# Optimization experiments

Hardware: AMD Instinct MI355X
Metric: run time of the kernel (lower is better)

The kernel has to match this reference:

```python
import jax, jax.numpy as jnp
import numpy as np

# Render constants matching GaussianRenderer(__init__): image size and top-K blend depth.
H, W, K = 128, 128, 10
N_G = 2048  # number of gaussians


def setup_inputs() -> dict:
    key = jax.random.key(0)
    k1, k2, k3, k4 = jax.random.split(key, 4)
    # Means in pixel coordinates so gaussians cover the image.
    gaussian_means = jax.random.uniform(k1, (N_G, 2), dtype=jnp.float32) * jnp.array([W, H], jnp.float32)
    # Rotation angle per gaussian in [0, 2pi).
    gaussian_rotations = jax.random.uniform(k2, (N_G,), dtype=jnp.float32) * (2.0 * np.pi)
    # log std-devs centered at log(3) => ~3px footprint.
    gaussian_log_scales = jax.random.normal(k3, (N_G, 2), dtype=jnp.float32) * 0.3 + np.log(3.0)
    gaussian_colors = jax.random.uniform(k4, (N_G, 3), dtype=jnp.float32)
    return {
        "gaussian_means": gaussian_means,
        "gaussian_rotations": gaussian_rotations,
        "gaussian_log_scales": gaussian_log_scales,
        "gaussian_colors": gaussian_colors,
    }


def reference(gaussian_means, gaussian_rotations, gaussian_log_scales, gaussian_colors):
    """2D Gaussian splatting: per-pixel top-K gaussians by opacity, alpha-composited.

    Covariance per gaussian: Sigma = R(theta) diag(exp(2*log_scales)) R(theta)^T.
    alpha_i(p) = exp(-0.5 * d^T Sigma^{-1} d), d = p - mean_i.
    Per pixel, the K gaussians with largest alpha are blended front-to-back:
        out = sum_i color_i * alpha_i * prod_{j<i} (1 - alpha_j).
    (The torch module's tile binning + max_G_per_tile is a GPU performance
    optimization; the dense evaluation here computes the same per-pixel math.)
    """
    cos_t = jnp.cos(gaussian_rotations)  # [N]
    sin_t = jnp.sin(gaussian_rotations)
    inv_var = jnp.exp(-2.0 * gaussian_log_scales)  # [N,2] = 1/sigma^2 per axis
    ivx, ivy = inv_var[:, 0], inv_var[:, 1]
    # Sigma^{-1} = R diag(1/sx^2, 1/sy^2) R^T  (symmetric 2x2: [[a, b], [b, c]])
    a = cos_t * cos_t * ivx + sin_t * sin_t * ivy  # [N]
    c = sin_t * sin_t * ivx + cos_t * cos_t * ivy
    b = cos_t * sin_t * (ivx - ivy)

    xs = jnp.arange(W, dtype=jnp.float32) + 0.5
    ys = jnp.arange(H, dtype=jnp.float32) + 0.5
    px, py = jnp.meshgrid(xs, ys)  # [H,W] each
    dx = px.reshape(-1, 1) - gaussian_means[:, 0]  # [P, N], P = H*W
    dy = py.reshape(-1, 1) - gaussian_means[:, 1]
    q = a * dx * dx + 2.0 * b * dx * dy + c * dy * dy  # Mahalanobis distance^2 [P,N]
    alpha = jnp.exp(-0.5 * q)  # [P,N] in (0,1]

    top_alpha, top_idx = jax.lax.top_k(alpha, K)  # [P,K], descending alpha
    # Front-to-back transmittance: T_0 = 1, T_i = prod_{j<i} (1 - alpha_j)
    trans = jnp.cumprod(1.0 - top_alpha, axis=1)
    trans = jnp.concatenate([jnp.ones_like(trans[:, :1]), trans[:, :-1]], axis=1)
    weight = top_alpha * trans  # [P,K]
    top_colors = gaussian_colors[top_idx]  # [P,K,3]
    image = jnp.einsum("pk,pkc->pc", weight, top_colors).reshape(H, W, 3)
    return image
```

## Files before the change

### kernel.cpp

```cpp
#include <hip/hip_runtime.h>

#define HH 128
#define WW 128
#define NPX (HH * WW)
#define KK 10
#define PXB 16
#define LCAP 352
#define JMAX 22
#define KEYC 6
#define SCAP (16 * KEYC)
#define SPAD (SCAP + 1)
#define ALPHA_MIN 5e-4f
#define RADIUS_K 3.8990f

typedef unsigned long long u64;
typedef unsigned int u32;

__global__ __launch_bounds__(256) void precompute_kernel(
    const float* __restrict__ means, const float* __restrict__ rots,
    const float* __restrict__ lscales, int nG,
    float4* __restrict__ bbox4, float4* __restrict__ prm4) {
  int g = blockIdx.x * blockDim.x + threadIdx.x;
  if (g >= nG) return;
  const float2* m2 = (const float2*)means;
  const float2* l2 = (const float2*)lscales;
  float2 mg = m2[g];
  float2 lg = l2[g];
  float smx = __expf(fmaxf(lg.x, lg.y));
  float r = fmaf(RADIUS_K * 1.01f, smx, 0.05f);
  float th = rots[g];
  float s = __sinf(th), c = __cosf(th);
  float ivx = __expf(-2.0f * lg.x);
  float ivy = __expf(-2.0f * lg.y);
  bbox4[g] = make_float4(mg.x, mg.y, r * r, mg.y);
  prm4[g] = make_float4(c * c * ivx + s * s * ivy,
                        2.0f * (c * s * (ivx - ivy)),
                        s * s * ivx + c * c * ivy, mg.x);
}

template <int NGC, bool PRE>
__global__ __launch_bounds__(256) void splat_kernel(
    const float* __restrict__ means, const float* __restrict__ rots,
    const float* __restrict__ lscales, const float* __restrict__ cols,
    const float4* __restrict__ bbox4, const float4* __restrict__ prm4,
    int nG_rt, float* __restrict__ out) {
  const int nG = NGC > 0 ? NGC : nG_rt;
  __shared__ float4 sA[LCAP];
  __shared__ float  sMy[LCAP];
  __shared__ int    glist[LCAP];
  __shared__ float2 sbuf[PXB][SPAD];
  __shared__ float2 wbuf[PXB][KK];
  __shared__ int    lcnt;

  int t = threadIdx.x;
  int lane = t & 63;
  int pl  = t >> 4;
  int tsl = t & 15;
  int tile = blockIdx.x;
  int x0 = (tile & 31) << 2, y0 = (tile >> 5) << 2;
  int x = x0 | (pl & 3), y = y0 | (pl >> 2);
  float px = (float)x + 0.5f, py = (float)y + 0.5f;

  if (t == 0) lcnt = 0;
  __syncthreads();

  const float2* m2 = (const float2*)means;
  const float2* l2 = (const float2*)lscales;
  float rx0 = (float)x0 + 0.5f, rx1 = (float)x0 + 3.5f;
  float ry0 = (float)y0 + 0.5f, ry1 = (float)y0 + 3.5f;
  for (int g = t; g < nG; g += 256) {
    bool hit;
    float4 bb;
    float2 mg, lg;
    if (PRE) {
      bb = bbox4[g];
      float cx = fminf(fmaxf(bb.x, rx0), rx1) - bb.x;
      float cy = fminf(fmaxf(bb.y, ry0), ry1) - bb.y;
      hit = (cx * cx + cy * cy <= bb.z);
    } else {
      mg = m2[g];
      lg = l2[g];
      float smx = __expf(fmaxf(lg.x, lg.y));
      float r = fmaf(RADIUS_K * 1.01f, smx, 0.05f);
      float cx = fminf(fmaxf(mg.x, rx0), rx1) - mg.x;
      float cy = fminf(fmaxf(mg.y, ry0), ry1) - mg.y;
      hit = (cx * cx + cy * cy <= r * r);
    }
    u64 mask = __ballot(hit);
    if (mask) {
      int leader = __ffsll((unsigned long long)mask) - 1;
      int base;
      if (lane == leader) base = atomicAdd(&lcnt, __popcll(mask));
      base = __shfl(base, leader);
      if (hit) {
        int idx = base + __popcll(mask & ((1ull << lane) - 1ull));
        if (idx < LCAP) {
          if (PRE) {
            sA[idx] = prm4[g];
            sMy[idx] = bb.w;
          } else {
            float th = rots[g];
            float s = __sinf(th), c = __cosf(th);
            float ivx = __expf(-2.0f * lg.x);
            float ivy = __expf(-2.0f * lg.y);
            sA[idx] = make_float4(c * c * ivx + s * s * ivy,
                                  2.0f * (c * s * (ivx - ivy)),
                                  s * s * ivx + c * c * ivy, mg.x);
            sMy[idx] = mg.y;
          }
          glist[idx] = g;
        }
      }
    }
  }
  __syncthreads();
  int cnt = min(lcnt, LCAP);
  int jcnt = (cnt + 15) >> 4;

  float ra[JMAX];
  float mymax = 0.0f;
#pragma unroll
  for (int j = 0; j < JMAX; ++j) {
    float a = 0.0f;
    if (j < jcnt) {
      int i = tsl + (j << 4);
      if (i < cnt) {
        float4 q0 = sA[i];
        float dx = px - q0.w, dy = py - sMy[i];
        float q = fmaf(dx, fmaf(q0.y, dy, q0.x * dx), q0.z * dy * dy);
        a = __expf(-0.5f * q);
      }
    }
    ra[j] = a;
    mymax = fmaxf(mymax, a);
  }

  float v = mymax;
#pragma unroll
  for (int k = 2; k <= 16; k <<= 1) {
#pragma unroll
    for (int j = k >> 1; j >= 1; j >>= 1) {
      float o = __shfl_xor(v, j, 16);
      bool keepMax = (((tsl & k) == 0) == ((tsl & j) == 0));
      v = keepMax ? fmaxf(v, o) : fminf(v, o);
    }
  }
  float tau = fmaxf(__shfl(v, 9, 16), ALPHA_MIN);

  int cpx = 0;
  int grp = lane >> 4;
#pragma unroll
  for (int j = 0; j < JMAX; ++j) {
    if (j < jcnt) {
      bool s = ra[j] >= tau;
      u64 mask = __ballot(s);
      u32 sub = (u32)((mask >> (grp * 16)) & 0xFFFFull);
      if (s) {
        int idx = cpx + __popc(sub & ((1u << tsl) - 1u));
        if (idx < SCAP)
          sbuf[pl][idx] = make_float2(ra[j], __int_as_float(glist[tsl + (j << 4)]));
      }
      cpx += __popc(sub);
    }
  }
  int scp = min(cpx, SCAP);
  int nw = min(scp, KK);

#pragma unroll
  for (int c = 0; c < KEYC; ++c) {
    if ((c << 4) < scp) {
      int i = tsl + (c << 4);
      u64 kc = 0;
      if (i < scp) {
        float2 e = sbuf[pl][i];
        kc = ((u64)__float_as_uint(e.x) << 32) | (u32)(~(u32)__float_as_int(e.y));
      }
      int rk = 0;
      for (int s2 = 0; s2 < scp; ++s2) {
        float2 e2 = sbuf[pl][s2];
        u64 ks2 = ((u64)__float_as_uint(e2.x) << 32) |
                  (u32)(~(u32)__float_as_int(e2.y));
        rk += (kc < ks2) ? 1 : 0;
      }
      if (kc != 0 && rk < KK)
        wbuf[pl][rk] = make_float2(__uint_as_float((u32)(kc >> 32)),
                                   __int_as_float((int)(~(u32)kc)));
    }
  }

  float my_alpha = 0.0f;
  int my_id = 0;
  if (tsl < nw) {
    float2 e = wbuf[pl][tsl];
    my_alpha = e.x;
    my_id = __float_as_int(e.y);
  }

  float T = 1.0f - my_alpha;
#pragma unroll
  for (int d = 1; d < 16; d <<= 1) {
    float u = __shfl_up(T, d, 16);
    if (tsl >= d) T *= u;
  }
  float ex = __shfl_up(T, 1, 16);
  if (tsl == 0) ex = 1.0f;
  float w = my_alpha * ex;
  float cr = 0.0f, cg = 0.0f, cb = 0.0f;
  if (my_alpha > 0.0f) {
    cr = w * cols[3 * my_id + 0];
    cg = w * cols[3 * my_id + 1];
    cb = w * cols[3 * my_id + 2];
  }
#pragma unroll
  for (int d = 1; d < 16; d <<= 1) {
    cr += __shfl_xor(cr, d);
    cg += __shfl_xor(cg, d);
    cb += __shfl_xor(cb, d);
  }
  int p = y * WW + x;
  if (tsl < 3) out[3 * p + tsl] = (tsl == 0) ? cr : ((tsl == 1) ? cg : cb);
}

extern "C" void kernel_launch(void* const* d_in, const int* in_sizes, int n_in,
                              void* d_out, int out_size, void* d_ws, size_t ws_size,
                              hipStream_t stream) {
  const float* means   = (const float*)d_in[0];
  const float* rots    = (const float*)d_in[1];
  const float* lscales = (const float*)d_in[2];
  const float* cols    = (const float*)d_in[3];
  float* out = (float*)d_out;
  int nG = in_sizes[1];

  size_t need = (size_t)nG * sizeof(float4) * 2;
  bool pre = (d_ws != nullptr) && (ws_size >= need);
  float4* bbox4 = (float4*)d_ws;
  float4* prm4 = (float4*)((char*)d_ws + (size_t)nG * sizeof(float4));

  if (pre)
    precompute_kernel<<<(nG + 255) / 256, 256, 0, stream>>>(means, rots,
                                                            lscales, nG,
                                                            bbox4, prm4);

  if (nG == 2048) {
    if (pre)
      splat_kernel<2048, true><<<NPX / PXB, 256, 0, stream>>>(
          means, rots, lscales, cols, bbox4, prm4, nG, out);
    else
      splat_kernel<2048, false><<<NPX / PXB, 256, 0, stream>>>(
          means, rots, lscales, cols, nullptr, nullptr, nG, out);
  } else {
    if (pre)
      splat_kernel<0, true><<<NPX / PXB, 256, 0, stream>>>(
          means, rots, lscales, cols, bbox4, prm4, nG, out);
    else
      splat_kernel<0, false><<<NPX / PXB, 256, 0, stream>>>(
          means, rots, lscales, cols, nullptr, nullptr, nG, out);
  }
}
```

Before: 70.21 us.

## Add coarse 16x16 tile binning pass to shrink per-tile gaussian scans

Replaces the per-gaussian precompute kernel with a coarse binning kernel. It launches 64 blocks, one per 16x16 pixel region, and each block writes a compacted list of the gaussians overlapping its region, along with their bounds and conic parameters. Each fine 4x4 splat block then culls only against its coarse region's list instead of scanning all gaussians. This cuts redundant global loads and bounds tests across the 1024 fine blocks. The cost is a much larger workspace (64 × nG × 32 bytes), and the code falls back to the slow, non-precomputed path if that workspace is not provided.

```diff
diff --git a/kernel.cpp b/kernel.cpp
--- a/kernel.cpp
+++ b/kernel.cpp
@@ -12,37 +12,64 @@
 #define SPAD (SCAP + 1)
 #define ALPHA_MIN 5e-4f
 #define RADIUS_K 3.8990f
+#define NCT 64
 
 typedef unsigned long long u64;
 typedef unsigned int u32;
 
-__global__ __launch_bounds__(256) void precompute_kernel(
+__global__ __launch_bounds__(256) void coarse_kernel(
     const float* __restrict__ means, const float* __restrict__ rots,
-    const float* __restrict__ lscales, int nG,
-    float4* __restrict__ bbox4, float4* __restrict__ prm4) {
-  int g = blockIdx.x * blockDim.x + threadIdx.x;
-  if (g >= nG) return;
+    const float* __restrict__ lscales, int nG, int cstride,
+    int* __restrict__ ccnt, float4* __restrict__ eb, float4* __restrict__ ep) {
+  __shared__ int lcnt;
+  int t = threadIdx.x;
+  int lane = t & 63;
+  if (t == 0) lcnt = 0;
+  __syncthreads();
+  int ct = blockIdx.x;
+  float rx0 = (float)((ct & 7) << 4) + 0.5f, rx1 = rx0 + 15.0f;
+  float ry0 = (float)((ct >> 3) << 4) + 0.5f, ry1 = ry0 + 15.0f;
   const float2* m2 = (const float2*)means;
   const float2* l2 = (const float2*)lscales;
-  float2 mg = m2[g];
-  float2 lg = l2[g];
-  float smx = __expf(fmaxf(lg.x, lg.y));
-  float r = fmaf(RADIUS_K * 1.01f, smx, 0.05f);
-  float th = rots[g];
-  float s = __sinf(th), c = __cosf(th);
-  float ivx = __expf(-2.0f * lg.x);
-  float ivy = __expf(-2.0f * lg.y);
-  bbox4[g] = make_float4(mg.x, mg.y, r * r, mg.y);
-  prm4[g] = make_float4(c * c * ivx + s * s * ivy,
-                        2.0f * (c * s * (ivx - ivy)),
-                        s * s * ivx + c * c * ivy, mg.x);
+  float4* ebt = eb + (size_t)ct * cstride;
+  float4* ept = ep + (size_t)ct * cstride;
+  for (int g = t; g < nG; g += 256) {
+    float2 mg = m2[g];
+    float2 lg = l2[g];
+    float smx = __expf(fmaxf(lg.x, lg.y));
+    float r = fmaf(RADIUS_K * 1.01f, smx, 0.05f);
+    float cx = fminf(fmaxf(mg.x, rx0), rx1) - mg.x;
+    float cy = fminf(fmaxf(mg.y, ry0), ry1) - mg.y;
+    bool hit = (cx * cx + cy * cy <= r * r);
+    u64 mask = __ballot(hit);
+    if (mask) {
+      int leader = __ffsll((unsigned long long)mask) - 1;
+      int base;
+      if (lane == leader) base = atomicAdd(&lcnt, __popcll(mask));
+      base = __shfl(base, leader);
+      if (hit) {
+        int idx = base + __popcll(mask & ((1ull << lane) - 1ull));
+        float th = rots[g];
+        float s = __sinf(th), c = __cosf(th);
+        float ivx = __expf(-2.0f * lg.x);
+        float ivy = __expf(-2.0f * lg.y);
+        ebt[idx] = make_float4(mg.x, mg.y, r * r, __int_as_float(g));
+        ept[idx] = make_float4(c * c * ivx + s * s * ivy,
+                               2.0f * (c * s * (ivx - ivy)),
+                               s * s * ivx + c * c * ivy, mg.x);
+      }
+    }
+  }
+  __syncthreads();
+  if (t == 0) ccnt[ct] = lcnt;
 }
 
 template <int NGC, bool PRE>
 __global__ __launch_bounds__(256) void splat_kernel(
     const float* __restrict__ means, const float* __restrict__ rots,
     const float* __restrict__ lscales, const float* __restrict__ cols,
-    const float4* __restrict__ bbox4, const float4* __restrict__ prm4,
+    const int* __restrict__ ccnt, const float4* __restrict__ eb,
+    const float4* __restrict__ ep, int cstride,
     int nG_rt, float* __restrict__ out) {
   const int nG = NGC > 0 ? NGC : nG_rt;
   __shared__ float4 sA[LCAP];
@@ -64,41 +91,54 @@
   if (t == 0) lcnt = 0;
   __syncthreads();
 
-  const float2* m2 = (const float2*)means;
-  const float2* l2 = (const float2*)lscales;
   float rx0 = (float)x0 + 0.5f, rx1 = (float)x0 + 3.5f;
   float ry0 = (float)y0 + 0.5f, ry1 = (float)y0 + 3.5f;
-  for (int g = t; g < nG; g += 256) {
-    bool hit;
-    float4 bb;
-    float2 mg, lg;
-    if (PRE) {
-      bb = bbox4[g];
-      float cx = fminf(fmaxf(bb.x, rx0), rx1) - bb.x;
-      float cy = fminf(fmaxf(bb.y, ry0), ry1) - bb.y;
-      hit = (cx * cx + cy * cy <= bb.z);
-    } else {
-      mg = m2[g];
-      lg = l2[g];
+  if (PRE) {
+    int ct = ((y0 >> 4) << 3) | (x0 >> 4);
+    int cc = ccnt[ct];
+    const float4* ebt = eb + (size_t)ct * cstride;
+    const float4* ept = ep + (size_t)ct * cstride;
+    for (int i = t; i < cc; i += 256) {
+      float4 b = ebt[i];
+      float cx = fminf(fmaxf(b.x, rx0), rx1) - b.x;
+      float cy = fminf(fmaxf(b.y, ry0), ry1) - b.y;
+      bool hit = (cx * cx + cy * cy <= b.z);
+      u64 mask = __ballot(hit);
+      if (mask) {
+        int leader = __ffsll((unsigned long long)mask) - 1;
+        int base;
+        if (lane == leader) base = atomicAdd(&lcnt, __popcll(mask));
+        base = __shfl(base, leader);
+        if (hit) {
+          int idx = base + __popcll(mask & ((1ull << lane) - 1ull));
+          if (idx < LCAP) {
+            sA[idx] = ept[i];
+            sMy[idx] = b.y;
+            glist[idx] = __float_as_int(b.w);
+          }
+        }
+      }
+    }
+  } else {
+    const float2* m2 = (const float2*)means;
+    const float2* l2 = (const float2*)lscales;
+    for (int g = t; g < nG; g += 256) {
+      float2 mg = m2[g];
+      float2 lg = l2[g];
       float smx = __expf(fmaxf(lg.x, lg.y));
       float r = fmaf(RADIUS_K * 1.01f, smx, 0.05f);
       float cx = fminf(fmaxf(mg.x, rx0), rx1) - mg.x;
       float cy = fminf(fmaxf(mg.y, ry0), ry1) - mg.y;
-      hit = (cx * cx + cy * cy <= r * r);
-    }
-    u64 mask = __ballot(hit);
-    if (mask) {
-      int leader = __ffsll((unsigned long long)mask) - 1;
-      int base;
-      if (lane == leader) base = atomicAdd(&lcnt, __popcll(mask));
-      base = __shfl(base, leader);
-      if (hit) {
-        int idx = base + __popcll(mask & ((1ull << lane) - 1ull));
-        if (idx < LCAP) {
-          if (PRE) {
-            sA[idx] = prm4[g];
-            sMy[idx] = bb.w;
-          } else {
+      bool hit = (cx * cx + cy * cy <= r * r);
+      u64 mask = __ballot(hit);
+      if (mask) {
+        int leader = __ffsll((unsigned long long)mask) - 1;
+        int base;
+        if (lane == leader) base = atomicAdd(&lcnt, __popcll(mask));
+        base = __shfl(base, leader);
+        if (hit) {
+          int idx = base + __popcll(mask & ((1ull << lane) - 1ull));
+          if (idx < LCAP) {
             float th = rots[g];
             float s = __sinf(th), c = __cosf(th);
             float ivx = __expf(-2.0f * lg.x);
@@ -107,8 +147,8 @@
                                   2.0f * (c * s * (ivx - ivy)),
                                   s * s * ivx + c * c * ivy, mg.x);
             sMy[idx] = mg.y;
+            glist[idx] = g;
           }
-          glist[idx] = g;
         }
       }
     }
@@ -231,29 +271,30 @@
   float* out = (float*)d_out;
   int nG = in_sizes[1];
 
-  size_t need = (size_t)nG * sizeof(float4) * 2;
+  int cstride = nG;
+  size_t need = 256 + (size_t)NCT * cstride * sizeof(float4) * 2;
   bool pre = (d_ws != nullptr) && (ws_size >= need);
-  float4* bbox4 = (float4*)d_ws;
-  float4* prm4 = (float4*)((char*)d_ws + (size_t)nG * sizeof(float4));
+  int* ccnt = (int*)d_ws;
+  float4* eb = (float4*)((char*)d_ws + 256);
+  float4* ep = eb + (size_t)NCT * cstride;
 
   if (pre)
-    precompute_kernel<<<(nG + 255) / 256, 256, 0, stream>>>(means, rots,
-                                                            lscales, nG,
-                                                            bbox4, prm4);
+    coarse_kernel<<<NCT, 256, 0, stream>>>(means, rots, lscales, nG, cstride,
+                                           ccnt, eb, ep);
 
   if (nG == 2048) {
     if (pre)
       splat_kernel<2048, true><<<NPX / PXB, 256, 0, stream>>>(
-          means, rots, lscales, cols, bbox4, prm4, nG, out);
+          means, rots, lscales, cols, ccnt, eb, ep, cstride, nG, out);
     else
       splat_kernel<2048, false><<<NPX / PXB, 256, 0, stream>>>(
-          means, rots, lscales, cols, nullptr, nullptr, nG, out);
+          means, rots, lscales, cols, nullptr, nullptr, nullptr, 0, nG, out);
   } else {
     if (pre)
       splat_kernel<0, true><<<NPX / PXB, 256, 0, stream>>>(
-          means, rots, lscales, cols, bbox4, prm4, nG, out);
+          means, rots, lscales, cols, ccnt, eb, ep, cstride, nG, out);
     else
       splat_kernel<0, false><<<NPX / PXB, 256, 0, stream>>>(
-          means, rots, lscales, cols, nullptr, nullptr, nG, out);
+          means, rots, lscales, cols, nullptr, nullptr, nullptr, 0, nG, out);
   }
 }
```

New measurement: 72.77 us. +3.6%, slower.
